# Kernel optimization log

Measured on AMD Instinct MI355X. Metric: run time of the kernel, lower is better.

Reference implementation:

```python
import jax, jax.numpy as jnp
import numpy as np

D1, D2, K = 2, 4, 2   # dilation1, dilation2, kernel_size
EPS = 1e-5            # BatchNorm eps (torch default)


def _dilated_nodes(queue, dilation, new_node):
    # queue: (L, bs, C, 1); take every `dilation`-th entry, append new node,
    # lay out as (bs, C, k) then flatten to (bs, C*k) matching torch's
    # cat(..., axis=2).reshape(bs, -1).
    nodes = jnp.concatenate([queue[0::dilation], new_node[None]], axis=0)  # (k, bs, C, 1)
    bs = new_node.shape[0]
    return jnp.moveaxis(nodes[..., 0], 0, -1).reshape(bs, -1)  # (bs, C*k)


def _bn_eval(h, scale, bias, mean, var):
    return (h - mean) * (scale * jax.lax.rsqrt(var + EPS)) + bias


def setup_inputs() -> dict:
    key = jax.random.key(0)
    ks = jax.random.split(key, 17)
    bs, din, mid, out = 16384, 512, 1024, 512
    in_ch = din * K          # 1024
    return {
        "x": jax.random.normal(ks[0], (bs, din, 1), jnp.float32),
        "conv1_queue": jax.random.normal(ks[1], (D1 * (K - 1), bs, din, 1), jnp.float32),
        "conv2_queue": jax.random.normal(ks[2], (D2 * (K - 1), bs, mid, 1), jnp.float32),
        "w1": jax.random.normal(ks[3], (mid, in_ch), jnp.float32) / np.sqrt(in_ch),
        "b1": jax.random.normal(ks[4], (mid,), jnp.float32) * 0.01,
        "w2": jax.random.normal(ks[5], (out, mid * K), jnp.float32) / np.sqrt(mid * K),
        "b2": jax.random.normal(ks[6], (out,), jnp.float32) * 0.01,
        "w_skip": jax.random.normal(ks[7], (out, in_ch), jnp.float32) / np.sqrt(in_ch),
        "b_skip": jax.random.normal(ks[8], (out,), jnp.float32) * 0.01,
        "bn1_scale": jax.random.uniform(ks[9], (mid,), jnp.float32, 0.5, 1.5),
        "bn1_bias": jax.random.normal(ks[10], (mid,), jnp.float32) * 0.01,
        "bn1_mean": jax.random.normal(ks[11], (mid,), jnp.float32) * 0.1,
        "bn1_var": jax.random.uniform(ks[12], (mid,), jnp.float32, 0.5, 1.5),
        "bn2_scale": jax.random.uniform(ks[13], (out,), jnp.float32, 0.5, 1.5),
        "bn2_bias": jax.random.normal(ks[14], (out,), jnp.float32) * 0.01,
        "bn2_mean": jax.random.normal(ks[15], (out,), jnp.float32) * 0.1,
        "bn2_var": jax.random.uniform(ks[16], (out,), jnp.float32, 0.5, 1.5),
    }


def reference(x, conv1_queue, conv2_queue, w1, b1, w2, b2, w_skip, b_skip,
              bn1_scale, bn1_bias, bn1_mean, bn1_var,
              bn2_scale, bn2_bias, bn2_mean, bn2_var):
    # l1_input: (bs, in_ch) = (bs, din*K)
    l1_input = _dilated_nodes(conv1_queue, D1, x)
    conv1_out = l1_input @ w1.T + b1                       # (bs, mid)
    conv1_out = _bn_eval(jax.nn.relu(conv1_out), bn1_scale, bn1_bias, bn1_mean, bn1_var)

    # l2_input: (bs, mid*K)
    l2_input = _dilated_nodes(conv2_queue, D2, conv1_out[:, :, None])
    conv2_out = l2_input @ w2.T + b2                       # (bs, out)
    conv2_out = conv2_out + (l1_input @ w_skip.T + b_skip)  # skip (in_ch != out_ch)
    conv2_out = jax.nn.relu(conv2_out)
    conv2_out = _bn_eval(conv2_out, bn2_scale, bn2_bias, bn2_mean, bn2_var)
    return conv2_out[:, :, None]                           # (bs, out, 1)
```

## Files before the change

kernel.cpp:

```cpp
#include <hip/hip_runtime.h>
#include <hip/hip_bf16.h>


#define BS   16384
#define DIN  512
#define MID  1024
#define NOUT 512
#define KA2  3072
#define BN_EPS 1e-5f

typedef __attribute__((ext_vector_type(8))) short bf16x8;
typedef __attribute__((ext_vector_type(4))) float floatx4;

#define GLDS(g, l) __builtin_amdgcn_global_load_lds( \
    (const __attribute__((address_space(1))) void*)(g), \
    (__attribute__((address_space(3))) void*)(l), 16, 0, 0)

__device__ __forceinline__ void cvt_store8(const float* __restrict__ src,
                                           __hip_bfloat16* __restrict__ dst) {
    float4 u = *(const float4*)src;
    float4 v = *(const float4*)(src + 4);
    __hip_bfloat16 tmp[8] __attribute__((aligned(16)));
    tmp[0] = __float2bfloat16(u.x); tmp[1] = __float2bfloat16(u.y);
    tmp[2] = __float2bfloat16(u.z); tmp[3] = __float2bfloat16(u.w);
    tmp[4] = __float2bfloat16(v.x); tmp[5] = __float2bfloat16(v.y);
    tmp[6] = __float2bfloat16(v.z); tmp[7] = __float2bfloat16(v.w);
    *(float4*)dst = *(const float4*)tmp;
}

__device__ __forceinline__ void cvt_store8_s2(const float* __restrict__ src,
                                              __hip_bfloat16* __restrict__ dst) {
    __hip_bfloat16 tmp[8] __attribute__((aligned(16)));
#pragma unroll
    for (int i = 0; i < 8; ++i) tmp[i] = __float2bfloat16(src[2 * i]);
    *(float4*)dst = *(const float4*)tmp;
}

#define T_Q2  ((long)BS * 128)
#define T_Q1X ((long)BS * 64)
#define T_W1  (1024L * 1024 / 8)
#define T_W2  (512L * 3072 / 8)
#define T_ALL (T_Q2 + T_Q1X + T_W1 + T_W2)

__global__ __launch_bounds__(256) void prep_all_kernel(
    const float* __restrict__ x, const float* __restrict__ q1,
    const float* __restrict__ q2, const float* __restrict__ w1,
    const float* __restrict__ w2, const float* __restrict__ wsk,
    __hip_bfloat16* __restrict__ A2,
    __hip_bfloat16* __restrict__ w1p, __hip_bfloat16* __restrict__ w2p)
{
    long id = (long)blockIdx.x * 256 + threadIdx.x;
    if (id < T_Q2) {
        long b = id >> 7;
        int j = (int)(id & 127) << 3;
        cvt_store8(q2 + b * MID + j, A2 + b * KA2 + j);
    } else if (id < T_Q2 + T_Q1X) {
        long id2 = id - T_Q2;
        long b = id2 >> 6;
        int j = (int)(id2 & 63) << 3;
        cvt_store8(q1 + b * DIN + j, A2 + b * KA2 + 2048 + j);
        cvt_store8(x  + b * DIN + j, A2 + b * KA2 + 2560 + j);
    } else if (id < T_Q2 + T_Q1X + T_W1) {
        long t = id - (T_Q2 + T_Q1X);
        long o8 = t * 8;
        int m = (int)(o8 >> 10), k0 = (int)(o8 & 1023);
        const float* src = w1 + m * 1024 + ((k0 < 512) ? 2 * k0 : 2 * (k0 - 512) + 1);
        cvt_store8_s2(src, w1p + o8);
    } else {
        long t = id - (T_Q2 + T_Q1X + T_W1);
        long o8 = t * 8;
        int o = (int)(o8 / 3072), k0 = (int)(o8 - (long)o * 3072);
        const float* src;
        if (k0 < 1024)      src = w2 + o * 2048 + 2 * k0;
        else if (k0 < 2048) src = w2 + o * 2048 + 2 * (k0 - 1024) + 1;
        else if (k0 < 2560) src = wsk + o * 1024 + 2 * (k0 - 2048);
        else                src = wsk + o * 1024 + 2 * (k0 - 2560) + 1;
        cvt_store8_s2(src, w2p + o8);
    }
}

template <int EPI>
__global__ __launch_bounds__(256) void mfma_gemm(
    const __hip_bfloat16* __restrict__ A, const __hip_bfloat16* __restrict__ B,
    int K, long strideA,
    const float* __restrict__ bias_a, const float* __restrict__ bias_b,
    const float* __restrict__ bn_s, const float* __restrict__ bn_b,
    const float* __restrict__ bn_m, const float* __restrict__ bn_v,
    __hip_bfloat16* __restrict__ hout, float* __restrict__ fout, int strideOut)
{
    __shared__ short As[128 * 32];
    __shared__ short Bs[128 * 32];

    const int t = threadIdx.x;
    const int lane = t & 63;
    const int wave = t >> 6;
    const int wm = wave >> 1, wn = wave & 1;

    const int p = blockIdx.x;
    const int m0 = ((p & 7) + 8 * ((p >> 3) & 15)) * 128;
    const int n0 = ((p >> 3) >> 4) * 128;

    floatx4 acc[4][4];
#pragma unroll
    for (int i = 0; i < 4; ++i)
#pragma unroll
        for (int j = 0; j < 4; ++j)
            acc[i][j] = (floatx4){0.f, 0.f, 0.f, 0.f};

    for (int k0 = 0; k0 < K; k0 += 32) {
#pragma unroll
        for (int c = 0; c < 2; ++c) {
            int fb = c * 256 + wave * 64;
            int f = fb + lane;
            GLDS(A + (size_t)(m0 + (f >> 2)) * strideA + k0 + (f & 3) * 8,
                 As + fb * 8);
            GLDS(B + (size_t)(n0 + (f >> 2)) * (size_t)K + k0 + (f & 3) * 8,
                 Bs + fb * 8);
        }
        __syncthreads();

        bf16x8 af[4], bfr[4];
#pragma unroll
        for (int i = 0; i < 4; ++i)
            af[i] = *(const bf16x8*)&As[(wm * 64 + i * 16 + (lane & 15)) * 32 +
                                        (lane >> 4) * 8];
#pragma unroll
        for (int j = 0; j < 4; ++j)
            bfr[j] = *(const bf16x8*)&Bs[(wn * 64 + j * 16 + (lane & 15)) * 32 +
                                         (lane >> 4) * 8];
#pragma unroll
        for (int i = 0; i < 4; ++i)
#pragma unroll
            for (int j = 0; j < 4; ++j)
                acc[i][j] = __builtin_amdgcn_mfma_f32_16x16x32_bf16(
                    af[i], bfr[j], acc[i][j], 0, 0, 0);
        __syncthreads();
    }

#pragma unroll
    for (int j = 0; j < 4; ++j) {
        int col = n0 + wn * 64 + j * 16 + (lane & 15);
        float bias = bias_a[col];
        if (EPI == 2) bias += bias_b[col];
        float scale = bn_s[col] * rsqrtf(bn_v[col] + BN_EPS);
        float mean = bn_m[col], beta = bn_b[col];
#pragma unroll
        for (int i = 0; i < 4; ++i) {
            int rbase = m0 + wm * 64 + i * 16 + (lane >> 4) * 4;
#pragma unroll
            for (int r = 0; r < 4; ++r) {
                float v = acc[i][j][r] + bias;
                v = fmaxf(v, 0.f);
                v = (v - mean) * scale + beta;
                if (EPI == 1)
                    hout[(size_t)(rbase + r) * strideOut + col] = __float2bfloat16(v);
                else
                    fout[(size_t)(rbase + r) * strideOut + col] = v;
            }
        }
    }
}

extern "C" void kernel_launch(void* const* d_in, const int* in_sizes, int n_in,
                              void* d_out, int out_size, void* d_ws, size_t ws_size,
                              hipStream_t stream) {
    const float* x   = (const float*)d_in[0];
    const float* q1  = (const float*)d_in[1];
    const float* q2  = (const float*)d_in[2];
    const float* w1  = (const float*)d_in[3];
    const float* b1  = (const float*)d_in[4];
    const float* w2  = (const float*)d_in[5];
    const float* b2  = (const float*)d_in[6];
    const float* wsk = (const float*)d_in[7];
    const float* bsk = (const float*)d_in[8];
    const float* s1  = (const float*)d_in[9];
    const float* bb1 = (const float*)d_in[10];
    const float* m1  = (const float*)d_in[11];
    const float* v1  = (const float*)d_in[12];
    const float* s2  = (const float*)d_in[13];
    const float* bb2 = (const float*)d_in[14];
    const float* m2  = (const float*)d_in[15];
    const float* v2  = (const float*)d_in[16];
    float* out = (float*)d_out;

    size_t needA2 = (size_t)BS * KA2 * sizeof(__hip_bfloat16);
    size_t needW  = ((size_t)1024 * 1024 + (size_t)512 * 3072) * sizeof(__hip_bfloat16);
    char* base;
    if (ws_size >= needA2 + needW)
        base = (char*)d_ws;
    else
        base = (char*)d_in[2] + (size_t)BS * MID * sizeof(float);
    __hip_bfloat16* A2  = (__hip_bfloat16*)base;
    __hip_bfloat16* w1p = (__hip_bfloat16*)(base + needA2);
    __hip_bfloat16* w2p = w1p + 1024 * 1024;

    prep_all_kernel<<<dim3((int)(T_ALL / 256)), dim3(256), 0, stream>>>(
        x, q1, q2, w1, w2, wsk, A2, w1p, w2p);

    mfma_gemm<1><<<dim3(1024), dim3(256), 0, stream>>>(
        A2 + 2048, w1p, 1024, KA2,
        b1, nullptr, s1, bb1, m1, v1,
        A2 + 1024, nullptr, KA2);

    mfma_gemm<2><<<dim3(512), dim3(256), 0, stream>>>(
        A2, w2p, 3072, KA2,
        b2, bsk, s2, bb2, m2, v2,
        nullptr, out, NOUT);
}
```

Measured before the change: 545.5 us.

## Replace first GEMM with 256x256 double-buffered 8-wave pipelined MFMA kernel

```diff
diff --git a/kernel.cpp b/kernel.cpp
--- a/kernel.cpp
+++ b/kernel.cpp
@@ -79,6 +79,132 @@
     }
 }
 
+
+#define PBAR() do { __builtin_amdgcn_sched_barrier(0); \
+                    __builtin_amdgcn_s_barrier(); \
+                    __builtin_amdgcn_sched_barrier(0); } while (0)
+#define LGKM0() asm volatile("s_waitcnt lgkmcnt(0)" ::: "memory")
+#define VMW(n)  asm volatile("s_waitcnt vmcnt(" #n ")" ::: "memory")
+
+#define STAGE_TILE(G, STRIDE, ROWBLK, K0, LBASE) do { \
+    _Pragma("unroll") for (int c_ = 0; c_ < 4; ++c_) { \
+        int f0_ = (c_ * 8 + wave) * 64; \
+        int f_  = f0_ + lane; \
+        int sr_ = f_ >> 3, cc_ = f_ & 7; \
+        GLDS((G) + (size_t)((ROWBLK) + sr_) * (STRIDE) + (K0) + ((cc_ ^ (sr_ & 7)) << 3), \
+             ((short*)(LBASE)) + f0_ * 8); \
+    } } while (0)
+
+#define READ_A(BUF, IH) do { \
+    _Pragma("unroll") for (int i_ = 0; i_ < 4; ++i_) { \
+        int r_ = wm * 128 + (IH) * 64 + i_ * 16 + (lane & 15); \
+        _Pragma("unroll") for (int kk_ = 0; kk_ < 2; ++kk_) { \
+            int cc_ = (kk_ * 4 + (lane >> 4)) ^ (r_ & 7); \
+            a[i_][kk_] = *(const bf16x8*)&As[BUF][r_][cc_ * 8]; \
+        } } } while (0)
+
+#define READ_B(BUF, JH) do { \
+    _Pragma("unroll") for (int j_ = 0; j_ < 2; ++j_) { \
+        int r_ = wn * 64 + (JH) * 32 + j_ * 16 + (lane & 15); \
+        _Pragma("unroll") for (int kk_ = 0; kk_ < 2; ++kk_) { \
+            int cc_ = (kk_ * 4 + (lane >> 4)) ^ (r_ & 7); \
+            b[(JH) * 2 + j_][kk_] = *(const bf16x8*)&Bs[BUF][r_][cc_ * 8]; \
+        } } } while (0)
+
+#define MFMA_Q(IH, JH) do { \
+    __builtin_amdgcn_s_setprio(1); \
+    _Pragma("unroll") for (int i_ = 0; i_ < 4; ++i_) \
+    _Pragma("unroll") for (int j_ = 0; j_ < 2; ++j_) \
+    _Pragma("unroll") for (int kk_ = 0; kk_ < 2; ++kk_) \
+        acc[(IH) * 4 + i_][(JH) * 2 + j_] = __builtin_amdgcn_mfma_f32_16x16x32_bf16( \
+            a[i_][kk_], b[(JH) * 2 + j_][kk_], acc[(IH) * 4 + i_][(JH) * 2 + j_], 0, 0, 0); \
+    __builtin_amdgcn_s_setprio(0); \
+} while (0)
+
+__global__ __launch_bounds__(512, 2) void gemm1_8ph(
+    const __hip_bfloat16* __restrict__ Ag,
+    const __hip_bfloat16* __restrict__ Bg,
+    const float* __restrict__ bias,
+    const float* __restrict__ bn_s, const float* __restrict__ bn_b,
+    const float* __restrict__ bn_m, const float* __restrict__ bn_v,
+    __hip_bfloat16* __restrict__ hout)
+{
+    __shared__ __align__(16) short As[2][256][64];
+    __shared__ __align__(16) short Bs[2][256][64];
+
+    const int t = threadIdx.x;
+    const int lane = t & 63;
+    const int wave = t >> 6;
+    const int wm = wave >> 2;
+    const int wn = wave & 3;
+
+    const int p = blockIdx.x;
+    const int m0 = ((p & 7) + 8 * ((p >> 3) & 7)) * 256;
+    const int n0 = (p >> 6) * 256;
+
+    floatx4 acc[8][4];
+#pragma unroll
+    for (int i = 0; i < 8; ++i)
+#pragma unroll
+        for (int j = 0; j < 4; ++j)
+            acc[i][j] = (floatx4){0.f, 0.f, 0.f, 0.f};
+
+    bf16x8 a[4][2], b[4][2];
+
+    STAGE_TILE(Bg, 1024, n0, 0,  Bs[0]);
+    STAGE_TILE(Ag, KA2,  m0, 0,  As[0]);
+    STAGE_TILE(Bg, 1024, n0, 64, Bs[1]);
+    STAGE_TILE(Ag, KA2,  m0, 64, As[1]);
+    VMW(0);
+    __builtin_amdgcn_s_barrier();
+
+    for (int it = 0; it < 8; ++it) {
+        const bool more = (it < 7);
+        const int kn = it * 128 + 128;
+
+        READ_A(0, 0); READ_B(0, 0);
+        PBAR(); LGKM0(); MFMA_Q(0, 0); PBAR();
+        READ_B(0, 1);
+        PBAR(); LGKM0(); MFMA_Q(0, 1); PBAR();
+        READ_A(0, 1);
+        if (more) STAGE_TILE(Bg, 1024, n0, kn, Bs[0]);
+        PBAR(); LGKM0(); MFMA_Q(1, 1); PBAR();
+        if (more) { VMW(4); } else { VMW(0); }
+        if (more) STAGE_TILE(Ag, KA2, m0, kn, As[0]);
+        PBAR(); MFMA_Q(1, 0); PBAR();
+
+        READ_A(1, 0); READ_B(1, 0);
+        PBAR(); LGKM0(); MFMA_Q(0, 0); PBAR();
+        READ_B(1, 1);
+        PBAR(); LGKM0(); MFMA_Q(0, 1); PBAR();
+        READ_A(1, 1);
+        if (more) STAGE_TILE(Bg, 1024, n0, kn + 64, Bs[1]);
+        PBAR(); LGKM0(); MFMA_Q(1, 1); PBAR();
+        VMW(4);
+        if (more) STAGE_TILE(Ag, KA2, m0, kn + 64, As[1]);
+        PBAR(); MFMA_Q(1, 0); PBAR();
+    }
+
+#pragma unroll
+    for (int j = 0; j < 4; ++j) {
+        int col = n0 + wn * 64 + j * 16 + (lane & 15);
+        float bias_v = bias[col];
+        float scale = bn_s[col] * rsqrtf(bn_v[col] + BN_EPS);
+        float mean = bn_m[col], beta = bn_b[col];
+#pragma unroll
+        for (int i = 0; i < 8; ++i) {
+            int rbase = m0 + wm * 128 + i * 16 + (lane >> 4) * 4;
+#pragma unroll
+            for (int r = 0; r < 4; ++r) {
+                float v = acc[i][j][r] + bias_v;
+                v = fmaxf(v, 0.f);
+                v = (v - mean) * scale + beta;
+                hout[(size_t)(rbase + r) * KA2 + col] = __float2bfloat16(v);
+            }
+        }
+    }
+}
+
 template <int EPI>
 __global__ __launch_bounds__(256) void mfma_gemm(
     const __hip_bfloat16* __restrict__ A, const __hip_bfloat16* __restrict__ B,
@@ -88,8 +214,8 @@
     const float* __restrict__ bn_m, const float* __restrict__ bn_v,
     __hip_bfloat16* __restrict__ hout, float* __restrict__ fout, int strideOut)
 {
-    __shared__ short As[128 * 32];
-    __shared__ short Bs[128 * 32];
+    __shared__ short Asl[128 * 32];
+    __shared__ short Bsl[128 * 32];
 
     const int t = threadIdx.x;
     const int lane = t & 63;
@@ -113,21 +239,21 @@
             int fb = c * 256 + wave * 64;
             int f = fb + lane;
             GLDS(A + (size_t)(m0 + (f >> 2)) * strideA + k0 + (f & 3) * 8,
-                 As + fb * 8);
+                 Asl + fb * 8);
             GLDS(B + (size_t)(n0 + (f >> 2)) * (size_t)K + k0 + (f & 3) * 8,
-                 Bs + fb * 8);
+                 Bsl + fb * 8);
         }
         __syncthreads();
 
         bf16x8 af[4], bfr[4];
 #pragma unroll
         for (int i = 0; i < 4; ++i)
-            af[i] = *(const bf16x8*)&As[(wm * 64 + i * 16 + (lane & 15)) * 32 +
-                                        (lane >> 4) * 8];
+            af[i] = *(const bf16x8*)&Asl[(wm * 64 + i * 16 + (lane & 15)) * 32 +
+                                         (lane >> 4) * 8];
 #pragma unroll
         for (int j = 0; j < 4; ++j)
-            bfr[j] = *(const bf16x8*)&Bs[(wn * 64 + j * 16 + (lane & 15)) * 32 +
-                                         (lane >> 4) * 8];
+            bfr[j] = *(const bf16x8*)&Bsl[(wn * 64 + j * 16 + (lane & 15)) * 32 +
+                                          (lane >> 4) * 8];
 #pragma unroll
         for (int i = 0; i < 4; ++i)
 #pragma unroll
@@ -197,10 +323,8 @@
     prep_all_kernel<<<dim3((int)(T_ALL / 256)), dim3(256), 0, stream>>>(
         x, q1, q2, w1, w2, wsk, A2, w1p, w2p);
 
-    mfma_gemm<1><<<dim3(1024), dim3(256), 0, stream>>>(
-        A2 + 2048, w1p, 1024, KA2,
-        b1, nullptr, s1, bb1, m1, v1,
-        A2 + 1024, nullptr, KA2);
+    gemm1_8ph<<<dim3(256), dim3(512), 0, stream>>>(
+        A2 + 2048, w1p, b1, s1, bb1, m1, v1, A2 + 1024);
 
     mfma_gemm<2><<<dim3(512), dim3(256), 0, stream>>>(
         A2, w2p, 3072, KA2,
```

New measurement: 539.4 us. Within noise of the previous version (-1.1%).
